# Optimization experiments

Measured on AMD Instinct MI355X. Metric: run time of the kernel, lower is better.

## Reference

```python
import jax, jax.numpy as jnp
import numpy as np

B, S, H, NH = 2, 2048, 1024, 16
HD = H // NH
BASE = 10000.0


def _rotate_half(x):
    x1, x2 = x[..., : x.shape[-1] // 2], x[..., x.shape[-1] // 2 :]
    return jnp.concatenate((-x2, x1), axis=-1)


def setup_inputs() -> dict:
    key = jax.random.key(0)
    ks = jax.random.split(key, 6)
    hidden_states = jax.random.normal(ks[0], (B, S, H), jnp.float32)
    scale = 0.02
    wq = jax.random.normal(ks[1], (H, H), jnp.float32) * scale
    wk = jax.random.normal(ks[2], (H, H), jnp.float32) * scale
    wv = jax.random.normal(ks[3], (H, H), jnp.float32) * scale
    wo = jax.random.normal(ks[4], (H, H), jnp.float32) * scale
    # additive causal mask, shape (B, 1, S, S): 0 on/below diagonal, large negative above
    neg = jnp.finfo(jnp.float32).min
    causal = jnp.where(jnp.tril(jnp.ones((S, S), dtype=bool)), 0.0, neg).astype(jnp.float32)
    attention_mask = jnp.broadcast_to(causal[None, None], (B, 1, S, S))
    position_ids = jnp.broadcast_to(jnp.arange(S, dtype=jnp.int32)[None], (B, S))
    return {
        "hidden_states": hidden_states,
        "attention_mask": attention_mask,
        "wq": wq,
        "wk": wk,
        "wv": wv,
        "wo": wo,
        "position_ids": position_ids,
    }


def reference(hidden_states, attention_mask, wq, wk, wv, wo, position_ids):
    b, s, h = hidden_states.shape
    dtype = hidden_states.dtype

    def proj(x, w):  # torch Linear: y = x @ w.T, then split heads -> (b, nh, s, hd)
        y = jnp.einsum("bsh,oh->bso", x, w)
        return y.reshape(b, s, NH, HD).transpose(0, 2, 1, 3)

    q = proj(hidden_states, wq)
    k = proj(hidden_states, wk)
    v = proj(hidden_states, wv)

    # rotary cache (computed in fp32 like torch), gathered by position_ids
    inv_freq = 1.0 / (BASE ** (jnp.arange(0, HD, 2, dtype=jnp.float32) / HD))
    t = jnp.arange(s, dtype=jnp.float32)
    freqs = jnp.outer(t, inv_freq)                  # (s, hd/2)
    emb = jnp.concatenate((freqs, freqs), axis=-1)  # (s, hd)
    pos = jnp.clip(position_ids, 0, s - 1)
    cos = jnp.cos(emb).astype(dtype)[pos][:, None]  # (b, 1, s, hd)
    sin = jnp.sin(emb).astype(dtype)[pos][:, None]

    q = q * cos + _rotate_half(q) * sin
    k = k * cos + _rotate_half(k) * sin

    scores = jnp.einsum("bhqd,bhkd->bhqk", q, k) / jnp.sqrt(jnp.asarray(HD, dtype))
    scores = scores + attention_mask
    attn = jax.nn.softmax(scores.astype(jnp.float32), axis=-1).astype(dtype)
    out = jnp.einsum("bhqk,bhkd->bhqd", attn, v)    # (b, nh, s, hd)
    out = out.transpose(0, 2, 1, 3).reshape(b, s, h)
    return jnp.einsum("bso,ho->bsh", out, wo)
```

## Files before the change

### kernel.cpp

```cpp
#include <hip/hip_runtime.h>
#include <cstdint>
#include <cstddef>

typedef unsigned short u16;
typedef __bf16 bf16x8 __attribute__((ext_vector_type(8)));
typedef float f32x4 __attribute__((ext_vector_type(4)));

constexpr int SEQ = 2048;
constexpr int HID = 1024;
constexpr int NHEAD = 16;
constexpr int HDIM = 64;

typedef __attribute__((address_space(1))) void gvoid;
typedef __attribute__((address_space(3))) void lvoid;

__device__ __forceinline__ u16 f2bf(float f) {
  union { float f; unsigned u; } v;
  v.f = f;
  unsigned r = v.u + 0x7fffu + ((v.u >> 16) & 1u);
  return (u16)(r >> 16);
}
__device__ __forceinline__ u16 f2bf_trunc(float f) {
  union { float f; unsigned u; } v;
  v.f = f;
  return (u16)(v.u >> 16);
}

__device__ __forceinline__ f32x4 mfma16(bf16x8 a, bf16x8 b, f32x4 c) {
  return __builtin_amdgcn_mfma_f32_16x16x32_bf16(a, b, c, 0, 0, 0);
}

__device__ __forceinline__ int detect_f32(const unsigned* __restrict__ hs) {
  unsigned w = hs[threadIdx.x & 63];
  u16 lo = (u16)(w & 0xffffu);
  int e = (lo >> 7) & 0xff;
  bool inr = (e >= 100 && e <= 154);
  unsigned long long m = __ballot(inr);
  return (__popcll(m) >= 48) ? 0 : 1;
}

__global__ __launch_bounds__(256) void cvt_kernel(
    const void* s0, const void* s1, const void* s2, const void* s3, const void* s4,
    u16* __restrict__ d0, u16* __restrict__ dW,
    float* __restrict__ cosb, float* __restrict__ sinb) {
  int b = blockIdx.x;
  if (b >= 4096) {
    int idx = (b - 4096) * 256 + threadIdx.x;
    int s = idx >> 5;
    int i = idx & 31;
    float inv_freq = expf(-(float)(2 * i) * (9.210340371976184f / 64.0f));
    float ang = (float)s * inv_freq;
    float c = cosf(ang), sn = sinf(ang);
    cosb[s * 64 + i]      = c;
    cosb[s * 64 + i + 32] = c;
    sinb[s * 64 + i]      = sn;
    sinb[s * 64 + i + 32] = sn;
    return;
  }
  const int is_f32 = detect_f32((const unsigned*)s0);
  const void* s; u16* d; long base;
  if (b < 2048) { s = s0; d = d0; base = (long)b * 2048; }
  else {
    int bb = b - 2048;
    int w = bb >> 9;
    base = (long)(bb & 511) * 2048;
    s = (w == 0) ? s1 : (w == 1) ? s2 : (w == 2) ? s3 : s4;
    d = dW + (long)w * 1048576;
  }
  long idx = base + (long)threadIdx.x * 8;
  if (is_f32) {
    const float* sf = (const float*)s;
    float4 a = *(const float4*)(sf + idx);
    float4 c = *(const float4*)(sf + idx + 4);
    ushort4 p0, p1;
    p0.x = f2bf(a.x); p0.y = f2bf(a.y); p0.z = f2bf(a.z); p0.w = f2bf(a.w);
    p1.x = f2bf(c.x); p1.y = f2bf(c.y); p1.z = f2bf(c.z); p1.w = f2bf(c.w);
    *(ushort4*)(d + idx) = p0;
    *(ushort4*)(d + idx + 4) = p1;
  } else {
    const u16* su = (const u16*)s;
    *(uint4*)(d + idx) = *(const uint4*)(su + idx);
  }
}

__device__ __forceinline__ void gemm_mainloop_128(
    const u16* __restrict__ Ag, const u16* __restrict__ Bg,
    int row0, int col0, f32x4 acc[4][4]) {
  __shared__ __align__(16) u16 As[128 * 64];
  __shared__ __align__(16) u16 Bs[128 * 64];
  const int t = threadIdx.x;
  const int lane = t & 63, wave = t >> 6;
  const int l15 = lane & 15, quad = lane >> 4;
  const int wm = wave >> 1, wn = wave & 1;
  const int cs = ((lane & 7) ^ ((lane >> 3) & 7)) * 8;
  const u16* aS = Ag + (size_t)(row0 + wave * 32 + (lane >> 3)) * 1024 + cs;
  const u16* bS = Bg + (size_t)(col0 + wave * 32 + (lane >> 3)) * 1024 + cs;
  const int swz0 = ((quad)     ^ (l15 & 7)) * 8;
  const int swz1 = ((4 + quad) ^ (l15 & 7)) * 8;

  for (int k0 = 0; k0 < 1024; k0 += 64) {
    __syncthreads();
#pragma unroll
    for (int j = 0; j < 4; j++) {
      __builtin_amdgcn_global_load_lds((gvoid*)(aS + k0 + j * 8192),
                                       (lvoid*)(As + wave * 2048 + j * 512), 16, 0, 0);
      __builtin_amdgcn_global_load_lds((gvoid*)(bS + k0 + j * 8192),
                                       (lvoid*)(Bs + wave * 2048 + j * 512), 16, 0, 0);
    }
    __syncthreads();
#pragma unroll
    for (int kk = 0; kk < 2; kk++) {
      const int sw = kk ? swz1 : swz0;
      bf16x8 af[4], bfr[4];
#pragma unroll
      for (int i = 0; i < 4; i++)
        af[i] = *(const bf16x8*)(As + (wm * 64 + i * 16 + l15) * 64 + sw);
#pragma unroll
      for (int j = 0; j < 4; j++)
        bfr[j] = *(const bf16x8*)(Bs + (wn * 64 + j * 16 + l15) * 64 + sw);
#pragma unroll
      for (int i = 0; i < 4; i++)
#pragma unroll
        for (int j = 0; j < 4; j++)
          acc[i][j] = mfma16(af[i], bfr[j], acc[i][j]);
    }
  }
}

__global__ __launch_bounds__(256) void qkv_kernel(
    const u16* __restrict__ X, const u16* __restrict__ Wcat,
    const int* __restrict__ pos_ids,
    const float* __restrict__ cosb, const float* __restrict__ sinb,
    u16* __restrict__ q_ws, u16* __restrict__ k_ws, u16* __restrict__ vt_ws) {
  const int row0 = blockIdx.x * 128;
  const int col0 = blockIdx.y * 128;
  const int z = col0 >> 10;
  f32x4 acc[4][4];
#pragma unroll
  for (int i = 0; i < 4; i++)
#pragma unroll
    for (int j = 0; j < 4; j++) acc[i][j] = f32x4{0.f, 0.f, 0.f, 0.f};

  gemm_mainloop_128(X, Wcat, row0, col0, acc);

  const int t = threadIdx.x;
  const int lane = t & 63, wave = t >> 6;
  const int l15 = lane & 15, quad = lane >> 4;
  const int wm = wave >> 1, wn = wave & 1;
  const int gr0 = row0 + wm * 64;
  const int gc0 = col0 + wn * 64;
  const int nh = (gc0 >> 6) & 15;
  const float qscale = (z == 0) ? 0.18033688011112042f : 1.0f;

  if (z < 2) {
    u16* dst = (z == 0) ? q_ws : k_ws;
#pragma unroll
    for (int i = 0; i < 4; i++) {
#pragma unroll
      for (int r = 0; r < 4; r++) {
        int m = gr0 + i * 16 + quad * 4 + r;
        int b = m >> 11, s = m & 2047;
        int p = pos_ids[m];
        p = min(max(p, 0), SEQ - 1);
#pragma unroll
        for (int j = 0; j < 4; j++) {
          int d = j * 16 + l15;
          float c = cosb[p * 64 + d];
          float sn = sinb[p * 64 + d];
          float v = acc[i][j][r];
          float partner = acc[i][j ^ 2][r];
          float rot = (j < 2) ? -partner : partner;
          float o = (v * c + rot * sn) * qscale;
          dst[((size_t)((b * NHEAD + nh) * SEQ + s) << 6) + d] = f2bf(o);
        }
      }
    }
  } else {
#pragma unroll
    for (int i = 0; i < 4; i++) {
      int m_base = gr0 + i * 16 + quad * 4;
      int b = m_base >> 11, s = m_base & 2047;
#pragma unroll
      for (int j = 0; j < 4; j++) {
        int d = j * 16 + l15;
        ushort4 pk;
        pk.x = f2bf(acc[i][j][0]);
        pk.y = f2bf(acc[i][j][1]);
        pk.z = f2bf(acc[i][j][2]);
        pk.w = f2bf(acc[i][j][3]);
        *(ushort4*)(vt_ws + ((size_t)((b * NHEAD + nh) * 64 + d)) * SEQ + s) = pk;
      }
    }
  }
}

__global__ __launch_bounds__(256) void attn_kernel(
    const u16* __restrict__ q_ws, const u16* __restrict__ k_ws,
    const u16* __restrict__ vt_ws, u16* __restrict__ attn_ws) {
  const int b = blockIdx.z;
  const int qt = b ? blockIdx.x : 15 - blockIdx.x;
  const int nh = blockIdx.y;
  const int bh = b * NHEAD + nh;
  __shared__ __align__(16) u16 Ks[2][128 * 64];
  __shared__ __align__(16) u16 Vts[2][64 * 128];
  __shared__ __align__(16) u16 Pl[128 * 64];

  const int t = threadIdx.x;
  const int lane = t & 63, wave = t >> 6;
  const int l15 = lane & 15, quad = lane >> 4;
  const int l7 = l15 & 7;
  const int wq0 = qt * 128 + wave * 32;

  bf16x8 aq[2][2];
#pragma unroll
  for (int i = 0; i < 2; i++) {
    const u16* qb = q_ws + ((size_t)bh * SEQ + wq0 + i * 16 + l15) * 64;
    aq[i][0] = *(const bf16x8*)(qb + quad * 8);
    aq[i][1] = *(const bf16x8*)(qb + 32 + quad * 8);
  }

  f32x4 O[2][4];
  float lp[2];
#pragma unroll
  for (int i = 0; i < 2; i++) {
    lp[i] = 0.f;
#pragma unroll
    for (int n = 0; n < 4; n++) O[i][n] = f32x4{0.f, 0.f, 0.f, 0.f};
  }

  const int krl = lane >> 3;
  const int kcs = ((lane & 7) ^ (krl & 7)) * 8;
  const u16* kS = k_ws + (size_t)bh * SEQ * 64 + (size_t)(wave * 32 + krl) * 64 + kcs;
  const int vrl = lane >> 4;
  const int vc4 = lane & 15;
  const u16* vS = vt_ws + (size_t)bh * 64 * SEQ + (size_t)(wave * 16 + vrl) * SEQ;
  int vx[4];
#pragma unroll
  for (int j = 0; j < 4; j++) vx[j] = (vc4 ^ ((4 * j + vrl) & 15)) * 8;

#define STAGE_KV(bi, kt_) do {                                                     \
    const size_t koff_ = (size_t)(kt_) * 8192;                                     \
    _Pragma("unroll")                                                              \
    for (int j = 0; j < 4; j++) {                                                  \
      __builtin_amdgcn_global_load_lds((gvoid*)(kS + koff_ + j * 512),             \
          (lvoid*)(&Ks[bi][0] + wave * 2048 + j * 512), 16, 0, 0);                 \
      __builtin_amdgcn_global_load_lds(                                            \
          (gvoid*)(vS + (size_t)j * 4 * SEQ + (kt_) * 128 + vx[j]),                \
          (lvoid*)(&Vts[bi][0] + wave * 2048 + j * 512), 16, 0, 0);                \
    }                                                                              \
  } while (0)

  const int nkt = qt + 1;
  STAGE_KV(0, 0);
  int cur = 0;
  for (int kt = 0; kt < nkt; ++kt) {
    if (kt + 1 < nkt) {
      STAGE_KV(cur ^ 1, kt + 1);
      asm volatile("s_waitcnt vmcnt(8)" ::: "memory");
    } else {
      asm volatile("s_waitcnt vmcnt(0)" ::: "memory");
    }
    __builtin_amdgcn_sched_barrier(0);
    __builtin_amdgcn_s_barrier();
    __builtin_amdgcn_sched_barrier(0);
    const u16* Ksb = &Ks[cur][0];
    const u16* Vtb = &Vts[cur][0];

#pragma unroll
    for (int h = 0; h < 2; h++) {
      f32x4 sc[2][4];
      __builtin_amdgcn_s_setprio(1);
#pragma unroll
      for (int ct = 0; ct < 4; ct++) {
        const u16* krow = Ksb + (h * 64 + ct * 16 + l15) * 64;
        bf16x8 bk0 = *(const bf16x8*)(krow + (quad ^ l7) * 8);
        bf16x8 bk1 = *(const bf16x8*)(krow + ((4 + quad) ^ l7) * 8);
#pragma unroll
        for (int i = 0; i < 2; i++) {
          f32x4 z = f32x4{0.f, 0.f, 0.f, 0.f};
          z = mfma16(bk0, aq[i][0], z);
          z = mfma16(bk1, aq[i][1], z);
          sc[i][ct] = z;
        }
      }
      __builtin_amdgcn_s_setprio(0);

      const int kbase = kt * 128 + h * 64;
      if (kt == qt) {
#pragma unroll
        for (int i = 0; i < 2; i++) {
          const int qrow = wq0 + i * 16 + l15;
          const int prow = (wave * 32 + i * 16 + l15) * 64;
#pragma unroll
          for (int ct = 0; ct < 4; ct++) {
            const int key0 = kbase + ct * 16 + quad * 4;
            float p[4];
#pragma unroll
            for (int r = 0; r < 4; r++) {
              float e = __builtin_amdgcn_exp2f(sc[i][ct][r]);
              if (key0 + r > qrow) e = 0.f;
              p[r] = e;
            }
            lp[i] += (p[0] + p[1]) + (p[2] + p[3]);
            ushort4 pk;
            pk.x = f2bf_trunc(p[0]); pk.y = f2bf_trunc(p[1]);
            pk.z = f2bf_trunc(p[2]); pk.w = f2bf_trunc(p[3]);
            *(ushort4*)&Pl[prow + ((ct * 2 + (quad >> 1)) ^ l7) * 8 + (quad & 1) * 4] = pk;
          }
        }
      } else {
#pragma unroll
        for (int i = 0; i < 2; i++) {
          const int prow = (wave * 32 + i * 16 + l15) * 64;
#pragma unroll
          for (int ct = 0; ct < 4; ct++) {
            float p[4];
#pragma unroll
            for (int r = 0; r < 4; r++) p[r] = __builtin_amdgcn_exp2f(sc[i][ct][r]);
            lp[i] += (p[0] + p[1]) + (p[2] + p[3]);
            ushort4 pk;
            pk.x = f2bf_trunc(p[0]); pk.y = f2bf_trunc(p[1]);
            pk.z = f2bf_trunc(p[2]); pk.w = f2bf_trunc(p[3]);
            *(ushort4*)&Pl[prow + ((ct * 2 + (quad >> 1)) ^ l7) * 8 + (quad & 1) * 4] = pk;
          }
        }
      }

      bf16x8 pa[2][2];
#pragma unroll
      for (int i = 0; i < 2; i++) {
        const u16* prow = Pl + (wave * 32 + i * 16 + l15) * 64;
        pa[i][0] = *(const bf16x8*)(prow + (quad ^ l7) * 8);
        pa[i][1] = *(const bf16x8*)(prow + ((4 + quad) ^ l7) * 8);
      }
      __builtin_amdgcn_s_setprio(1);
#pragma unroll
      for (int n = 0; n < 4; n++) {
        const u16* vrow = Vtb + (n * 16 + l15) * 128;
        bf16x8 bv0 = *(const bf16x8*)(vrow + ((h * 8 + quad) ^ l15) * 8);
        bf16x8 bv1 = *(const bf16x8*)(vrow + ((h * 8 + 4 + quad) ^ l15) * 8);
#pragma unroll
        for (int i = 0; i < 2; i++) {
          O[i][n] = mfma16(pa[i][0], bv0, O[i][n]);
          O[i][n] = mfma16(pa[i][1], bv1, O[i][n]);
        }
      }
      __builtin_amdgcn_s_setprio(0);
    }

    __builtin_amdgcn_sched_barrier(0);
    __builtin_amdgcn_s_barrier();
    __builtin_amdgcn_sched_barrier(0);
    cur ^= 1;
  }
#undef STAGE_KV

#pragma unroll
  for (int i = 0; i < 2; i++) {
    float l = lp[i];
    l += __shfl_xor(l, 16, 64);
    l += __shfl_xor(l, 32, 64);
#pragma unroll
    for (int r = 0; r < 4; r++) {
      float inv = 1.0f / __shfl(l, quad * 4 + r, 64);
      int q = wq0 + i * 16 + quad * 4 + r;
      size_t base = ((size_t)(b * SEQ + q)) * HID + nh * 64;
#pragma unroll
      for (int n = 0; n < 4; n++)
        attn_ws[base + n * 16 + l15] = f2bf(O[i][n][r] * inv);
    }
  }
}

__global__ __launch_bounds__(256) void out_proj_kernel(
    const u16* __restrict__ A, const u16* __restrict__ Wo, void* __restrict__ out,
    const unsigned* __restrict__ hs_raw) {
  __shared__ __align__(16) u16 As[64 * 64];
  __shared__ __align__(16) u16 Bs[128 * 64];
  const int row0 = blockIdx.x * 64;
  const int col0 = blockIdx.y * 128;
  const int is_f32 = detect_f32(hs_raw);
  const int t = threadIdx.x;
  const int lane = t & 63, wave = t >> 6;
  const int l15 = lane & 15, quad = lane >> 4;
  const int wm = wave >> 1, wn = wave & 1;
  const int cs = ((lane & 7) ^ ((lane >> 3) & 7)) * 8;
  const u16* aS = A  + (size_t)(row0 + wave * 16 + (lane >> 3)) * 1024 + cs;
  const u16* bS = Wo + (size_t)(col0 + wave * 32 + (lane >> 3)) * 1024 + cs;
  const int swz0 = ((quad)     ^ (l15 & 7)) * 8;
  const int swz1 = ((4 + quad) ^ (l15 & 7)) * 8;

  f32x4 acc[2][4];
#pragma unroll
  for (int i = 0; i < 2; i++)
#pragma unroll
    for (int j = 0; j < 4; j++) acc[i][j] = f32x4{0.f, 0.f, 0.f, 0.f};

  for (int k0 = 0; k0 < 1024; k0 += 64) {
    __syncthreads();
#pragma unroll
    for (int j = 0; j < 2; j++)
      __builtin_amdgcn_global_load_lds((gvoid*)(aS + k0 + j * 8192),
                                       (lvoid*)(As + wave * 1024 + j * 512), 16, 0, 0);
#pragma unroll
    for (int j = 0; j < 4; j++)
      __builtin_amdgcn_global_load_lds((gvoid*)(bS + k0 + j * 8192),
                                       (lvoid*)(Bs + wave * 2048 + j * 512), 16, 0, 0);
    __syncthreads();
#pragma unroll
    for (int kk = 0; kk < 2; kk++) {
      const int sw = kk ? swz1 : swz0;
      bf16x8 af[2], bfr[4];
#pragma unroll
      for (int i = 0; i < 2; i++)
        af[i] = *(const bf16x8*)(As + (wm * 32 + i * 16 + l15) * 64 + sw);
#pragma unroll
      for (int j = 0; j < 4; j++)
        bfr[j] = *(const bf16x8*)(Bs + (wn * 64 + j * 16 + l15) * 64 + sw);
#pragma unroll
      for (int i = 0; i < 2; i++)
#pragma unroll
        for (int j = 0; j < 4; j++)
          acc[i][j] = mfma16(af[i], bfr[j], acc[i][j]);
    }
  }

  const int gr0 = row0 + wm * 32;
  const int gc0 = col0 + wn * 64;
#pragma unroll
  for (int i = 0; i < 2; i++)
#pragma unroll
    for (int r = 0; r < 4; r++) {
      int m = gr0 + i * 16 + quad * 4 + r;
      if (is_f32) {
        float* o = (float*)out;
#pragma unroll
        for (int j = 0; j < 4; j++)
          o[(size_t)m * 1024 + gc0 + j * 16 + l15] = acc[i][j][r];
      } else {
        u16* o = (u16*)out;
#pragma unroll
        for (int j = 0; j < 4; j++)
          o[(size_t)m * 1024 + gc0 + j * 16 + l15] = f2bf(acc[i][j][r]);
      }
    }
}

extern "C" void kernel_launch(void* const* d_in, const int* in_sizes, int n_in,
                              void* d_out, int out_size, void* d_ws, size_t ws_size,
                              hipStream_t stream) {
  const void* hs = d_in[0];
  const void* wq = d_in[2];
  const void* wk = d_in[3];
  const void* wv = d_in[4];
  const void* wo = d_in[5];
  const int* pos = (const int*)d_in[6];

  char* ws = (char*)d_ws;
  float* cosb = (float*)ws;
  float* sinb = (float*)(ws + (512 << 10));
  u16* xbf    = (u16*)(ws + (1 << 20));
  u16* wcat   = xbf + (size_t)4194304;
  u16* q_ws   = wcat + (size_t)4 * 1048576;
  u16* k_ws   = q_ws + (size_t)2 * NHEAD * SEQ * HDIM;
  u16* vt_ws  = k_ws + (size_t)2 * NHEAD * SEQ * HDIM;
  u16* attn_ws = vt_ws + (size_t)2 * NHEAD * SEQ * HDIM;

  cvt_kernel<<<4352, 256, 0, stream>>>(hs, wq, wk, wv, wo, xbf, wcat, cosb, sinb);
  qkv_kernel<<<dim3(32, 24), 256, 0, stream>>>(xbf, wcat, pos, cosb, sinb,
                                               q_ws, k_ws, vt_ws);
  attn_kernel<<<dim3(16, NHEAD, 2), 256, 0, stream>>>(q_ws, k_ws, vt_ws, attn_ws);
  out_proj_kernel<<<dim3(64, 8), 256, 0, stream>>>(attn_ws, wcat + (size_t)3 * 1048576,
                                                   d_out, (const unsigned*)hs);
}
```

Measured before the change: 196.2 us.

## Double-buffer LDS tiles in QKV and output projection GEMM mainloops

Both projection GEMM loops now keep two LDS buffers per operand. The next K-slice is prefetched with global_load_lds while MFMA runs on the current one, using partial vmcnt waits and raw s_barrier with sched barriers. This is meant to hide global-to-LDS latency that the old load-sync-compute loop exposed. It doubles LDS use per block (64KB in the QKV kernel), which can lower occupancy.

```diff
diff --git a/kernel.cpp b/kernel.cpp
--- a/kernel.cpp
+++ b/kernel.cpp
@@ -86,8 +86,8 @@
 __device__ __forceinline__ void gemm_mainloop_128(
     const u16* __restrict__ Ag, const u16* __restrict__ Bg,
     int row0, int col0, f32x4 acc[4][4]) {
-  __shared__ __align__(16) u16 As[128 * 64];
-  __shared__ __align__(16) u16 Bs[128 * 64];
+  __shared__ __align__(16) u16 As[2][128 * 64];
+  __shared__ __align__(16) u16 Bs[2][128 * 64];
   const int t = threadIdx.x;
   const int lane = t & 63, wave = t >> 6;
   const int l15 = lane & 15, quad = lane >> 4;
@@ -98,33 +98,52 @@
   const int swz0 = ((quad)     ^ (l15 & 7)) * 8;
   const int swz1 = ((4 + quad) ^ (l15 & 7)) * 8;
 
+#define STAGE_AB(bi, k0_) do {                                                   \
+    _Pragma("unroll")                                                            \
+    for (int j = 0; j < 4; j++) {                                                \
+      __builtin_amdgcn_global_load_lds((gvoid*)(aS + (k0_) + j * 8192),          \
+          (lvoid*)(&As[bi][0] + wave * 2048 + j * 512), 16, 0, 0);               \
+      __builtin_amdgcn_global_load_lds((gvoid*)(bS + (k0_) + j * 8192),          \
+          (lvoid*)(&Bs[bi][0] + wave * 2048 + j * 512), 16, 0, 0);               \
+    }                                                                            \
+  } while (0)
+
+  STAGE_AB(0, 0);
+  int cur = 0;
   for (int k0 = 0; k0 < 1024; k0 += 64) {
-    __syncthreads();
-#pragma unroll
-    for (int j = 0; j < 4; j++) {
-      __builtin_amdgcn_global_load_lds((gvoid*)(aS + k0 + j * 8192),
-                                       (lvoid*)(As + wave * 2048 + j * 512), 16, 0, 0);
-      __builtin_amdgcn_global_load_lds((gvoid*)(bS + k0 + j * 8192),
-                                       (lvoid*)(Bs + wave * 2048 + j * 512), 16, 0, 0);
-    }
-    __syncthreads();
+    if (k0 + 64 < 1024) {
+      STAGE_AB(cur ^ 1, k0 + 64);
+      asm volatile("s_waitcnt vmcnt(8)" ::: "memory");
+    } else {
+      asm volatile("s_waitcnt vmcnt(0)" ::: "memory");
+    }
+    __builtin_amdgcn_sched_barrier(0);
+    __builtin_amdgcn_s_barrier();
+    __builtin_amdgcn_sched_barrier(0);
+    const u16* Asb = &As[cur][0];
+    const u16* Bsb = &Bs[cur][0];
 #pragma unroll
     for (int kk = 0; kk < 2; kk++) {
       const int sw = kk ? swz1 : swz0;
       bf16x8 af[4], bfr[4];
 #pragma unroll
       for (int i = 0; i < 4; i++)
-        af[i] = *(const bf16x8*)(As + (wm * 64 + i * 16 + l15) * 64 + sw);
+        af[i] = *(const bf16x8*)(Asb + (wm * 64 + i * 16 + l15) * 64 + sw);
 #pragma unroll
       for (int j = 0; j < 4; j++)
-        bfr[j] = *(const bf16x8*)(Bs + (wn * 64 + j * 16 + l15) * 64 + sw);
+        bfr[j] = *(const bf16x8*)(Bsb + (wn * 64 + j * 16 + l15) * 64 + sw);
 #pragma unroll
       for (int i = 0; i < 4; i++)
 #pragma unroll
         for (int j = 0; j < 4; j++)
           acc[i][j] = mfma16(af[i], bfr[j], acc[i][j]);
     }
-  }
+    __builtin_amdgcn_sched_barrier(0);
+    __builtin_amdgcn_s_barrier();
+    __builtin_amdgcn_sched_barrier(0);
+    cur ^= 1;
+  }
+#undef STAGE_AB
 }
 
 __global__ __launch_bounds__(256) void qkv_kernel(
@@ -375,8 +394,8 @@
 __global__ __launch_bounds__(256) void out_proj_kernel(
     const u16* __restrict__ A, const u16* __restrict__ Wo, void* __restrict__ out,
     const unsigned* __restrict__ hs_raw) {
-  __shared__ __align__(16) u16 As[64 * 64];
-  __shared__ __align__(16) u16 Bs[128 * 64];
+  __shared__ __align__(16) u16 As[2][64 * 64];
+  __shared__ __align__(16) u16 Bs[2][128 * 64];
   const int row0 = blockIdx.x * 64;
   const int col0 = blockIdx.y * 128;
   const int is_f32 = detect_f32(hs_raw);
@@ -396,34 +415,53 @@
 #pragma unroll
     for (int j = 0; j < 4; j++) acc[i][j] = f32x4{0.f, 0.f, 0.f, 0.f};
 
+#define STAGE_OP(bi, k0_) do {                                                   \
+    _Pragma("unroll")                                                            \
+    for (int j = 0; j < 2; j++)                                                  \
+      __builtin_amdgcn_global_load_lds((gvoid*)(aS + (k0_) + j * 8192),          \
+          (lvoid*)(&As[bi][0] + wave * 1024 + j * 512), 16, 0, 0);               \
+    _Pragma("unroll")                                                            \
+    for (int j = 0; j < 4; j++)                                                  \
+      __builtin_amdgcn_global_load_lds((gvoid*)(bS + (k0_) + j * 8192),          \
+          (lvoid*)(&Bs[bi][0] + wave * 2048 + j * 512), 16, 0, 0);               \
+  } while (0)
+
+  STAGE_OP(0, 0);
+  int cur = 0;
   for (int k0 = 0; k0 < 1024; k0 += 64) {
-    __syncthreads();
-#pragma unroll
-    for (int j = 0; j < 2; j++)
-      __builtin_amdgcn_global_load_lds((gvoid*)(aS + k0 + j * 8192),
-                                       (lvoid*)(As + wave * 1024 + j * 512), 16, 0, 0);
-#pragma unroll
-    for (int j = 0; j < 4; j++)
-      __builtin_amdgcn_global_load_lds((gvoid*)(bS + k0 + j * 8192),
-                                       (lvoid*)(Bs + wave * 2048 + j * 512), 16, 0, 0);
-    __syncthreads();
+    if (k0 + 64 < 1024) {
+      STAGE_OP(cur ^ 1, k0 + 64);
+      asm volatile("s_waitcnt vmcnt(6)" ::: "memory");
+    } else {
+      asm volatile("s_waitcnt vmcnt(0)" ::: "memory");
+    }
+    __builtin_amdgcn_sched_barrier(0);
+    __builtin_amdgcn_s_barrier();
+    __builtin_amdgcn_sched_barrier(0);
+    const u16* Asb = &As[cur][0];
+    const u16* Bsb = &Bs[cur][0];
 #pragma unroll
     for (int kk = 0; kk < 2; kk++) {
       const int sw = kk ? swz1 : swz0;
       bf16x8 af[2], bfr[4];
 #pragma unroll
       for (int i = 0; i < 2; i++)
-        af[i] = *(const bf16x8*)(As + (wm * 32 + i * 16 + l15) * 64 + sw);
+        af[i] = *(const bf16x8*)(Asb + (wm * 32 + i * 16 + l15) * 64 + sw);
 #pragma unroll
       for (int j = 0; j < 4; j++)
-        bfr[j] = *(const bf16x8*)(Bs + (wn * 64 + j * 16 + l15) * 64 + sw);
+        bfr[j] = *(const bf16x8*)(Bsb + (wn * 64 + j * 16 + l15) * 64 + sw);
 #pragma unroll
       for (int i = 0; i < 2; i++)
 #pragma unroll
         for (int j = 0; j < 4; j++)
           acc[i][j] = mfma16(af[i], bfr[j], acc[i][j]);
     }
-  }
+    __builtin_amdgcn_sched_barrier(0);
+    __builtin_amdgcn_s_barrier();
+    __builtin_amdgcn_sched_barrier(0);
+    cur ^= 1;
+  }
+#undef STAGE_OP
 
   const int gr0 = row0 + wm * 32;
   const int gc0 = col0 + wn * 64;
```

After: 197.8 us. Within noise of the previous version (+0.8%).
